# Kernel optimization log

Measured on AMD Instinct MI355X. Metric: run time of the kernel, lower is better.

## Reference

```python
import jax, jax.numpy as jnp
import numpy as np

SEQDIM = 512      # hidden-state dim of h
EMBED_DIM = 512   # attention embedding dim
VFEAT_DIM = 384   # visual feature channels (must equal VFEAT_LEN for the broadcast in the original code)
VFEAT_LEN = 384   # number of visual regions


def setup_inputs() -> dict:
    key = jax.random.key(0)
    k_h, k_v, k_wh, k_wv, k_wg = jax.random.split(key, 5)
    h = jax.random.normal(k_h, (SEQDIM, 1), dtype=jnp.float32)
    v = jax.random.normal(k_v, (VFEAT_DIM, VFEAT_LEN), dtype=jnp.float32)
    wh = jax.random.normal(k_wh, (VFEAT_LEN, EMBED_DIM), dtype=jnp.float32) * 0.05
    wv = jax.random.normal(k_wv, (EMBED_DIM, VFEAT_DIM), dtype=jnp.float32) * 0.05
    wg = jax.random.normal(k_wg, (EMBED_DIM, SEQDIM), dtype=jnp.float32) * 0.05
    return {"h": h, "v": v, "wh": wh, "wv": wv, "wg": wg}


def reference(h, v, wh, wv, wg):
    # s = W_v V + (W_g h_t) 1^T  -> (embed_dim, vfeat_len)
    s = jnp.matmul(wv, v) + jnp.matmul(wg, h)  # (E, L) + (E, 1) broadcasts == outer product with ones row
    # z = w_h tanh(s)            -> (vfeat_len, vfeat_len)
    z = jnp.matmul(wh, jnp.tanh(s))
    alpha = jax.nn.softmax(z, axis=-1)
    # v (D, L) * alpha[..., None] (L, L, 1) -> broadcast to (L, D, L) with D == L
    weighted_avg = v * alpha[..., None]
    return weighted_avg
```

## Files before the change

kernel.cpp:

```cpp
#include <hip/hip_runtime.h>
#include <hip/hip_bf16.h>

#define SDIM 512
#define EDIM 512
#define LDIM 384
#define DDIM 384

typedef __attribute__((ext_vector_type(4))) float float4v;

__global__ __launch_bounds__(384) void k_tanh_s(
    const float* __restrict__ h, const float* __restrict__ v,
    const float* __restrict__ wv, const float* __restrict__ wg,
    float* __restrict__ t)
{
    const int e   = blockIdx.x;
    const int tid = threadIdx.x;
    __shared__ float wvs[DDIM];
    __shared__ float red[6];

    float acc = 0.f;
    for (int k = tid; k < SDIM; k += 384)
        acc += wg[e * SDIM + k] * h[k];
    for (int off = 32; off > 0; off >>= 1)
        acc += __shfl_down(acc, off, 64);
    if ((tid & 63) == 0) red[tid >> 6] = acc;

    wvs[tid] = wv[e * DDIM + tid];
    __syncthreads();

    const float gh = red[0] + red[1] + red[2] + red[3] + red[4] + red[5];

    const float* vp = v + tid;
    float a0 = 0.f, a1 = 0.f, a2 = 0.f, a3 = 0.f;
    #pragma unroll 4
    for (int k = 0; k < DDIM; k += 4) {
        a0 += wvs[k]     * vp[(k)     * LDIM];
        a1 += wvs[k + 1] * vp[(k + 1) * LDIM];
        a2 += wvs[k + 2] * vp[(k + 2) * LDIM];
        a3 += wvs[k + 3] * vp[(k + 3) * LDIM];
    }
    t[e * LDIM + tid] = tanhf((a0 + a1) + (a2 + a3) + gh);
}

__global__ __launch_bounds__(384) void k_softmax(
    const float* __restrict__ wh, const float* __restrict__ t,
    float* __restrict__ alpha)
{
    const int r   = blockIdx.x;
    const int tid = threadIdx.x;
    __shared__ float whs[EDIM];
    __shared__ float redm[6];
    __shared__ float reds[6];

    for (int e = tid; e < EDIM; e += 384)
        whs[e] = wh[r * EDIM + e];
    __syncthreads();

    const float* tp = t + tid;
    float a0 = 0.f, a1 = 0.f, a2 = 0.f, a3 = 0.f;
    #pragma unroll 4
    for (int e = 0; e < EDIM; e += 4) {
        a0 += whs[e]     * tp[(e)     * LDIM];
        a1 += whs[e + 1] * tp[(e + 1) * LDIM];
        a2 += whs[e + 2] * tp[(e + 2) * LDIM];
        a3 += whs[e + 3] * tp[(e + 3) * LDIM];
    }
    const float z = (a0 + a1) + (a2 + a3);

    float m = z;
    for (int off = 32; off > 0; off >>= 1)
        m = fmaxf(m, __shfl_down(m, off, 64));
    if ((tid & 63) == 0) redm[tid >> 6] = m;
    __syncthreads();
    m = fmaxf(fmaxf(fmaxf(redm[0], redm[1]), fmaxf(redm[2], redm[3])),
              fmaxf(redm[4], redm[5]));

    const float ez = expf(z - m);

    float s = ez;
    for (int off = 32; off > 0; off >>= 1)
        s += __shfl_down(s, off, 64);
    if ((tid & 63) == 0) reds[tid >> 6] = s;
    __syncthreads();
    const float rs = 1.f / (((reds[0] + reds[1]) + (reds[2] + reds[3]))
                            + (reds[4] + reds[5]));

    alpha[r * LDIM + tid] = ez * rs;
}

__global__ __launch_bounds__(384) void k_out(
    const float* __restrict__ v, const float* __restrict__ alpha,
    float* __restrict__ out)
{
    constexpr int VPS = (LDIM * DDIM) / 4;
    const int i = blockIdx.x >> 2;
    const int q = blockIdx.x & 3;

    __shared__ float arow[DDIM];
    arow[threadIdx.x] = alpha[i * DDIM + threadIdx.x];
    __syncthreads();

    const int jb  = (int)threadIdx.x / 96;
    const int col = (int)threadIdx.x % 96;
    const int j0  = q * 96;

    const float4v* v4 = (const float4v*)v;
    float4v* o4 = (float4v*)out + (size_t)i * VPS;

    #pragma unroll 6
    for (int it = 0; it < 24; ++it) {
        const int j   = j0 + it * 4 + jb;
        const int idx = j * 96 + col;
        o4[idx] = v4[idx] * arow[j];
    }
}

extern "C" void kernel_launch(void* const* d_in, const int* in_sizes, int n_in,
                              void* d_out, int out_size, void* d_ws, size_t ws_size,
                              hipStream_t stream)
{
    const float* h  = (const float*)d_in[0];
    const float* v  = (const float*)d_in[1];
    const float* wh = (const float*)d_in[2];
    const float* wv = (const float*)d_in[3];
    const float* wg = (const float*)d_in[4];
    float* out = (float*)d_out;

    float* t     = (float*)d_ws;
    float* alpha = t + EDIM * LDIM;

    k_tanh_s <<<EDIM, 384, 0, stream>>>(h, v, wv, wg, t);
    k_softmax<<<LDIM, 384, 0, stream>>>(wh, t, alpha);
    k_out    <<<4 * LDIM, 384, 0, stream>>>(v, alpha, out);
}
```

Measured before the change: 261.8 us.

## Compute two rows per block in GEMV stages and tile output kernel for v reuse

The tanh and softmax kernels now process two output rows per block, so each loaded column of v or t feeds two accumulators and is read half as often. Loads are batched 16 at a time to raise memory-level parallelism. The output kernel is retiled so each block keeps a 24-row slice of v in registers and writes it scaled for 16 different alpha rows, which removes repeated v reads. In exchange the GEMV grids shrink to 256 and 192 blocks, which may leave compute units underused, and register pressure rises.

```diff
diff --git a/kernel.cpp b/kernel.cpp
--- a/kernel.cpp
+++ b/kernel.cpp
@@ -13,105 +13,149 @@
     const float* __restrict__ wv, const float* __restrict__ wg,
     float* __restrict__ t)
 {
-    const int e   = blockIdx.x;
+    const int e0  = blockIdx.x * 2;
     const int tid = threadIdx.x;
-    __shared__ float wvs[DDIM];
-    __shared__ float red[6];
+    __shared__ float wvs0[DDIM], wvs1[DDIM];
+    __shared__ float red[2][6];
 
-    float acc = 0.f;
-    for (int k = tid; k < SDIM; k += 384)
-        acc += wg[e * SDIM + k] * h[k];
-    for (int off = 32; off > 0; off >>= 1)
-        acc += __shfl_down(acc, off, 64);
-    if ((tid & 63) == 0) red[tid >> 6] = acc;
+    float g0 = 0.f, g1 = 0.f;
+    for (int k = tid; k < SDIM; k += 384) {
+        const float hk = h[k];
+        g0 += wg[e0 * SDIM + k] * hk;
+        g1 += wg[(e0 + 1) * SDIM + k] * hk;
+    }
+    for (int off = 32; off > 0; off >>= 1) {
+        g0 += __shfl_down(g0, off, 64);
+        g1 += __shfl_down(g1, off, 64);
+    }
+    if ((tid & 63) == 0) { red[0][tid >> 6] = g0; red[1][tid >> 6] = g1; }
 
-    wvs[tid] = wv[e * DDIM + tid];
+    wvs0[tid] = wv[e0 * DDIM + tid];
+    wvs1[tid] = wv[(e0 + 1) * DDIM + tid];
     __syncthreads();
 
-    const float gh = red[0] + red[1] + red[2] + red[3] + red[4] + red[5];
+    const float gh0 = ((red[0][0] + red[0][1]) + (red[0][2] + red[0][3]))
+                      + (red[0][4] + red[0][5]);
+    const float gh1 = ((red[1][0] + red[1][1]) + (red[1][2] + red[1][3]))
+                      + (red[1][4] + red[1][5]);
 
     const float* vp = v + tid;
-    float a0 = 0.f, a1 = 0.f, a2 = 0.f, a3 = 0.f;
-    #pragma unroll 4
-    for (int k = 0; k < DDIM; k += 4) {
-        a0 += wvs[k]     * vp[(k)     * LDIM];
-        a1 += wvs[k + 1] * vp[(k + 1) * LDIM];
-        a2 += wvs[k + 2] * vp[(k + 2) * LDIM];
-        a3 += wvs[k + 3] * vp[(k + 3) * LDIM];
+    float a[4] = {0.f, 0.f, 0.f, 0.f};
+    float b[4] = {0.f, 0.f, 0.f, 0.f};
+    for (int kb = 0; kb < DDIM; kb += 16) {
+        float vv[16];
+        #pragma unroll
+        for (int u = 0; u < 16; ++u)
+            vv[u] = vp[(kb + u) * LDIM];
+        #pragma unroll
+        for (int u = 0; u < 16; ++u) {
+            a[u & 3] += wvs0[kb + u] * vv[u];
+            b[u & 3] += wvs1[kb + u] * vv[u];
+        }
     }
-    t[e * LDIM + tid] = tanhf((a0 + a1) + (a2 + a3) + gh);
+    t[e0 * LDIM + tid]       = tanhf((a[0] + a[1]) + (a[2] + a[3]) + gh0);
+    t[(e0 + 1) * LDIM + tid] = tanhf((b[0] + b[1]) + (b[2] + b[3]) + gh1);
 }
 
 __global__ __launch_bounds__(384) void k_softmax(
     const float* __restrict__ wh, const float* __restrict__ t,
     float* __restrict__ alpha)
 {
-    const int r   = blockIdx.x;
+    const int r0  = blockIdx.x * 2;
     const int tid = threadIdx.x;
-    __shared__ float whs[EDIM];
-    __shared__ float redm[6];
-    __shared__ float reds[6];
+    __shared__ float whs0[EDIM], whs1[EDIM];
+    __shared__ float redm[2][6], reds[2][6];
 
-    for (int e = tid; e < EDIM; e += 384)
-        whs[e] = wh[r * EDIM + e];
+    for (int e = tid; e < EDIM; e += 384) {
+        whs0[e] = wh[r0 * EDIM + e];
+        whs1[e] = wh[(r0 + 1) * EDIM + e];
+    }
     __syncthreads();
 
     const float* tp = t + tid;
-    float a0 = 0.f, a1 = 0.f, a2 = 0.f, a3 = 0.f;
-    #pragma unroll 4
-    for (int e = 0; e < EDIM; e += 4) {
-        a0 += whs[e]     * tp[(e)     * LDIM];
-        a1 += whs[e + 1] * tp[(e + 1) * LDIM];
-        a2 += whs[e + 2] * tp[(e + 2) * LDIM];
-        a3 += whs[e + 3] * tp[(e + 3) * LDIM];
+    float a[4] = {0.f, 0.f, 0.f, 0.f};
+    float b[4] = {0.f, 0.f, 0.f, 0.f};
+    for (int eb = 0; eb < EDIM; eb += 16) {
+        float tv[16];
+        #pragma unroll
+        for (int u = 0; u < 16; ++u)
+            tv[u] = tp[(eb + u) * LDIM];
+        #pragma unroll
+        for (int u = 0; u < 16; ++u) {
+            a[u & 3] += whs0[eb + u] * tv[u];
+            b[u & 3] += whs1[eb + u] * tv[u];
+        }
     }
-    const float z = (a0 + a1) + (a2 + a3);
+    const float z0 = (a[0] + a[1]) + (a[2] + a[3]);
+    const float z1 = (b[0] + b[1]) + (b[2] + b[3]);
 
-    float m = z;
-    for (int off = 32; off > 0; off >>= 1)
-        m = fmaxf(m, __shfl_down(m, off, 64));
-    if ((tid & 63) == 0) redm[tid >> 6] = m;
+    float m0 = z0, m1 = z1;
+    for (int off = 32; off > 0; off >>= 1) {
+        m0 = fmaxf(m0, __shfl_down(m0, off, 64));
+        m1 = fmaxf(m1, __shfl_down(m1, off, 64));
+    }
+    if ((tid & 63) == 0) { redm[0][tid >> 6] = m0; redm[1][tid >> 6] = m1; }
     __syncthreads();
-    m = fmaxf(fmaxf(fmaxf(redm[0], redm[1]), fmaxf(redm[2], redm[3])),
-              fmaxf(redm[4], redm[5]));
+    m0 = fmaxf(fmaxf(fmaxf(redm[0][0], redm[0][1]), fmaxf(redm[0][2], redm[0][3])),
+               fmaxf(redm[0][4], redm[0][5]));
+    m1 = fmaxf(fmaxf(fmaxf(redm[1][0], redm[1][1]), fmaxf(redm[1][2], redm[1][3])),
+               fmaxf(redm[1][4], redm[1][5]));
 
-    const float ez = expf(z - m);
+    const float e0 = expf(z0 - m0);
+    const float e1 = expf(z1 - m1);
 
-    float s = ez;
-    for (int off = 32; off > 0; off >>= 1)
-        s += __shfl_down(s, off, 64);
-    if ((tid & 63) == 0) reds[tid >> 6] = s;
+    float s0 = e0, s1 = e1;
+    for (int off = 32; off > 0; off >>= 1) {
+        s0 += __shfl_down(s0, off, 64);
+        s1 += __shfl_down(s1, off, 64);
+    }
+    if ((tid & 63) == 0) { reds[0][tid >> 6] = s0; reds[1][tid >> 6] = s1; }
     __syncthreads();
-    const float rs = 1.f / (((reds[0] + reds[1]) + (reds[2] + reds[3]))
-                            + (reds[4] + reds[5]));
+    const float rs0 = 1.f / (((reds[0][0] + reds[0][1]) + (reds[0][2] + reds[0][3]))
+                             + (reds[0][4] + reds[0][5]));
+    const float rs1 = 1.f / (((reds[1][0] + reds[1][1]) + (reds[1][2] + reds[1][3]))
+                             + (reds[1][4] + reds[1][5]));
 
-    alpha[r * LDIM + tid] = ez * rs;
+    alpha[r0 * LDIM + tid]       = e0 * rs0;
+    alpha[(r0 + 1) * LDIM + tid] = e1 * rs1;
 }
 
-__global__ __launch_bounds__(384) void k_out(
+__global__ __launch_bounds__(256) void k_out(
     const float* __restrict__ v, const float* __restrict__ alpha,
     float* __restrict__ out)
 {
     constexpr int VPS = (LDIM * DDIM) / 4;
-    const int i = blockIdx.x >> 2;
-    const int q = blockIdx.x & 3;
+    const int jt = blockIdx.x & 15;
+    const int it = blockIdx.x >> 4;
+    const int j0 = jt * 24;
+    const int i0 = it * 16;
+    const int tid = (int)threadIdx.x;
 
-    __shared__ float arow[DDIM];
-    arow[threadIdx.x] = alpha[i * DDIM + threadIdx.x];
+    __shared__ float al[16][24];
+    for (int x = tid; x < 16 * 24; x += 256) {
+        const int ii = x / 24;
+        const int jj = x - ii * 24;
+        al[ii][jj] = alpha[(i0 + ii) * LDIM + j0 + jj];
+    }
+
+    const float4v* v4 = (const float4v*)v;
+    float4v vr[9];
+    int jj[9];
+    #pragma unroll
+    for (int k = 0; k < 9; ++k) {
+        const int x = k * 256 + tid;
+        vr[k] = v4[j0 * 96 + x];
+        jj[k] = x / 96;
+    }
     __syncthreads();
 
-    const int jb  = (int)threadIdx.x / 96;
-    const int col = (int)threadIdx.x % 96;
-    const int j0  = q * 96;
-
-    const float4v* v4 = (const float4v*)v;
-    float4v* o4 = (float4v*)out + (size_t)i * VPS;
-
-    #pragma unroll 6
-    for (int it = 0; it < 24; ++it) {
-        const int j   = j0 + it * 4 + jb;
-        const int idx = j * 96 + col;
-        o4[idx] = v4[idx] * arow[j];
+    float4v* o4 = (float4v*)out;
+    size_t base = (size_t)i0 * VPS + j0 * 96;
+    for (int ii = 0; ii < 16; ++ii) {
+        #pragma unroll
+        for (int k = 0; k < 9; ++k)
+            o4[base + k * 256 + tid] = vr[k] * al[ii][jj[k]];
+        base += VPS;
     }
 }
 
@@ -129,7 +173,7 @@
     float* t     = (float*)d_ws;
     float* alpha = t + EDIM * LDIM;
 
-    k_tanh_s <<<EDIM, 384, 0, stream>>>(h, v, wv, wg, t);
-    k_softmax<<<LDIM, 384, 0, stream>>>(wh, t, alpha);
-    k_out    <<<4 * LDIM, 384, 0, stream>>>(v, alpha, out);
+    k_tanh_s <<<EDIM / 2, 384, 0, stream>>>(h, v, wv, wg, t);
+    k_softmax<<<LDIM / 2, 384, 0, stream>>>(wh, t, alpha);
+    k_out    <<<16 * 24, 256, 0, stream>>>(v, alpha, out);
 }
```

After: 262.0 us. Within noise of the previous version (+0.1%).
